# Kernel optimization log

Measured on AMD Instinct MI355X. Metric: run time of the kernel, lower is better.

## Reference

```python
import jax, jax.numpy as jnp
import numpy as np

B, SQ, SK, D, H, DFF, L = 8, 1024, 1024, 512, 8, 2048, 2
HD = D // H  # head dim = 64
EPS = 1e-5


def _ln(x, g, b):
    mu = jnp.mean(x, axis=-1, keepdims=True)
    var = jnp.mean((x - mu) ** 2, axis=-1, keepdims=True)
    return (x - mu) * jax.lax.rsqrt(var + EPS) * g + b


def setup_inputs() -> dict:
    key = jax.random.key(0)
    ks = jax.random.split(key, 16)
    std = 0.02
    inp = {
        'q': jax.random.normal(ks[0], (B, SQ, D), jnp.float32),
        'k': jax.random.normal(ks[1], (B, SK, D), jnp.float32),
        'v': jax.random.normal(ks[2], (B, SK, D), jnp.float32),
        # per-layer stacked params (weights stored [in, out])
        'WQ': jax.random.normal(ks[3], (L, D, D), jnp.float32) * std,
        'bQ': jnp.zeros((L, D), jnp.float32),
        'WK': jax.random.normal(ks[4], (L, D, D), jnp.float32) * std,
        'bK': jnp.zeros((L, D), jnp.float32),
        'WV': jax.random.normal(ks[5], (L, D, D), jnp.float32) * std,
        'bV': jnp.zeros((L, D), jnp.float32),
        'WO': jax.random.normal(ks[6], (L, D, D), jnp.float32) * std,
        'bO': jnp.zeros((L, D), jnp.float32),
        'Wf1': jax.random.normal(ks[7], (L, D, DFF), jnp.float32) * std,
        'bf1': jnp.zeros((L, DFF), jnp.float32),
        'Wf2': jax.random.normal(ks[8], (L, DFF, D), jnp.float32) * std,
        'bf2': jnp.zeros((L, D), jnp.float32),
        'ln1_g': jnp.ones((L, D), jnp.float32),
        'ln1_b': jnp.zeros((L, D), jnp.float32),
        'ln2_g': jnp.ones((L, D), jnp.float32),
        'ln2_b': jnp.zeros((L, D), jnp.float32),
        'scale': jnp.full((L,), HD ** -0.5, jnp.float32),       # self.scale init
        'extra_scale': jnp.ones((L,), jnp.float32),             # self.extra_scale init
        'gate_attn': jnp.ones((L,), jnp.float32),
        'gate_ffn': jnp.ones((L,), jnp.float32),
    }
    return inp


def reference(q, k, v, WQ, bQ, WK, bK, WV, bV, WO, bO, Wf1, bf1, Wf2, bf2,
              ln1_g, ln1_b, ln2_g, ln2_b, scale, extra_scale, gate_attn, gate_ffn):
    prev = None  # Realformer residual attention scores
    for i in range(L):
        # QKV projections -> [B, H, S, HD]
        qh = (jnp.einsum('bsd,de->bse', q, WQ[i]) + bQ[i]).reshape(B, SQ, H, HD).transpose(0, 2, 1, 3)
        kh = (jnp.einsum('bsd,de->bse', k, WK[i]) + bK[i]).reshape(B, SK, H, HD).transpose(0, 2, 1, 3)
        vh = (jnp.einsum('bsd,de->bse', v, WV[i]) + bV[i]).reshape(B, SK, H, HD).transpose(0, 2, 1, 3)
        eff_scale = scale[i] * jnp.clip(extra_scale[i], 0.01, 50.0)
        scores = jnp.einsum('bhqd,bhkd->bhqk', qh, kh) * eff_scale  # [B,H,SQ,SK]
        if prev is not None:
            scores = scores + prev
        attn = jax.nn.softmax(scores, axis=-1)
        out = jnp.einsum('bhqk,bhkd->bhqd', attn, vh)
        out = out.transpose(0, 2, 1, 3).reshape(B, SQ, D)
        out = jnp.einsum('bsd,de->bse', out, WO[i]) + bO[i]
        # gated residual + post-norm
        q = q + jax.nn.softplus(gate_attn[i]) * out
        q = _ln(q, ln1_g[i], ln1_b[i])
        # FFN (exact gelu like torch default)
        ff = jax.nn.gelu(jnp.einsum('bsd,df->bsf', q, Wf1[i]) + bf1[i], approximate=False)
        ff = jnp.einsum('bsf,fd->bsd', ff, Wf2[i]) + bf2[i]
        q = q + jax.nn.softplus(gate_ffn[i]) * ff
        q = _ln(q, ln2_g[i], ln2_b[i])
        prev = scores
    return q
```

## Files before the change

### kernel.cpp

```cpp
#include <hip/hip_runtime.h>

#define B_   8
#define SQ_  1024
#define SK_  1024
#define D_   512
#define H_   8
#define DFF_ 2048
#define L_   2
#define HD_  64
#define M_   8192

typedef __bf16 bf16;
using bf16x8 = __attribute__((ext_vector_type(8))) __bf16;
using f32x4  = __attribute__((ext_vector_type(4))) float;

__device__ inline f32x4 mfma16(bf16x8 a, bf16x8 b, f32x4 c) {
  return __builtin_amdgcn_mfma_f32_16x16x32_bf16(a, b, c, 0, 0, 0);
}

__device__ __forceinline__ void gl2lds16(const bf16* g, bf16* l) {
  __builtin_amdgcn_global_load_lds(
      (const __attribute__((address_space(1))) void*)g,
      (__attribute__((address_space(3))) void*)l, 16, 0, 0);
}

__global__ __launch_bounds__(256) void transpose_k(
    const float* __restrict__ in, bf16* __restrict__ out, int R, int C) {
  __shared__ bf16 tile[32][33];
  const float* inp  = in  + (size_t)blockIdx.z * R * C;
  bf16*        outp = out + (size_t)blockIdx.z * R * C;
  int c0 = blockIdx.x * 32, r0 = blockIdx.y * 32;
  int tx = threadIdx.x & 31, ty = threadIdx.x >> 5;
#pragma unroll
  for (int i = 0; i < 32; i += 8)
    tile[ty + i][tx] = (bf16)inp[(size_t)(r0 + ty + i) * C + c0 + tx];
  __syncthreads();
#pragma unroll
  for (int i = 0; i < 32; i += 8)
    outp[(size_t)(c0 + ty + i) * R + r0 + tx] = tile[tx][ty + i];
}

__global__ __launch_bounds__(256) void f2b_k(const float* __restrict__ in,
                                             bf16* __restrict__ out, int n) {
  int i = (blockIdx.x * 256 + threadIdx.x) * 4;
  if (i < n) {
    float4 v = *(const float4*)&in[i];
    out[i] = (bf16)v.x; out[i + 1] = (bf16)v.y;
    out[i + 2] = (bf16)v.z; out[i + 3] = (bf16)v.w;
  }
}

template<int BN>
__global__ __launch_bounds__(256) void gemm_t(
    const bf16* __restrict__ A, const bf16* __restrict__ Bt,
    const float* __restrict__ bias, bf16* __restrict__ Cb,
    float* __restrict__ Cf, int Nsz, int Ksz, int gelu) {
  constexpr int NI = BN / 32;
  __shared__ bf16 As[2][128 * 32];
  __shared__ bf16 Bs[2][BN * 32];
  const int tid = threadIdx.x;
  const int m0 = blockIdx.x * 128, n0 = blockIdx.y * BN;
  const int w = tid >> 6, lane = tid & 63, quad = lane >> 4, l16 = lane & 15;
  const int wm = (w & 1) << 6, wn = (w >> 1) * (BN / 2);
  const int r4 = lane >> 2;
  const int k8 = (lane & 3) * 8;
  f32x4 acc[4][NI] = {};

  auto stage = [&](int k0, int buf) {
    gl2lds16(&A[(size_t)(m0 + w * 16 + r4) * Ksz + k0 + k8],
             &As[buf][(w * 16) * 32]);
    gl2lds16(&A[(size_t)(m0 + (w + 4) * 16 + r4) * Ksz + k0 + k8],
             &As[buf][((w + 4) * 16) * 32]);
    gl2lds16(&Bt[(size_t)(n0 + w * 16 + r4) * Ksz + k0 + k8],
             &Bs[buf][(w * 16) * 32]);
    if constexpr (BN == 128)
      gl2lds16(&Bt[(size_t)(n0 + (w + 4) * 16 + r4) * Ksz + k0 + k8],
               &Bs[buf][((w + 4) * 16) * 32]);
  };

  stage(0, 0);
  __syncthreads();
  int buf = 0;
  for (int k0 = 0; k0 < Ksz; k0 += 32, buf ^= 1) {
    if (k0 + 32 < Ksz) stage(k0 + 32, buf ^ 1);
    bf16x8 af[4], bfr[NI];
#pragma unroll
    for (int i = 0; i < 4; i++)
      af[i] = *(const bf16x8*)&As[buf][(wm + i * 16 + l16) * 32 + quad * 8];
#pragma unroll
    for (int i = 0; i < NI; i++)
      bfr[i] = *(const bf16x8*)&Bs[buf][(wn + i * 16 + l16) * 32 + quad * 8];
#pragma unroll
    for (int mi = 0; mi < 4; mi++)
#pragma unroll
      for (int ni = 0; ni < NI; ni++)
        acc[mi][ni] = mfma16(af[mi], bfr[ni], acc[mi][ni]);
    __syncthreads();
  }
#pragma unroll
  for (int mi = 0; mi < 4; mi++)
#pragma unroll
    for (int ni = 0; ni < NI; ni++) {
      int col = n0 + wn + ni * 16 + l16;
      float bv = bias[col];
#pragma unroll
      for (int r = 0; r < 4; r++) {
        int row = m0 + wm + mi * 16 + quad * 4 + r;
        float x = acc[mi][ni][r] + bv;
        if (gelu) x = 0.5f * x * (1.0f + erff(x * 0.70710678118f));
        size_t idx = (size_t)row * Nsz + col;
        if (Cb) Cb[idx] = (bf16)x;
        if (Cf) Cf[idx] = x;
      }
    }
}

__global__ __launch_bounds__(256) void vtrans_k(const bf16* __restrict__ vh,
                                                int vstride, int coloff,
                                                bf16* __restrict__ vt) {
  __shared__ bf16 sm[64][72];
  int kt = blockIdx.x, bh = blockIdx.y;
  int b = bh >> 3, h = bh & 7;
  int tid = threadIdx.x;
  for (int c = tid; c < 512; c += 256) {
    int key = c >> 3, off = (c & 7) * 8;
    *(uint4*)&sm[key][off] = *(const uint4*)
        &vh[(size_t)(b * SK_ + kt * 64 + key) * vstride + coloff + h * 64 + off];
  }
  __syncthreads();
  for (int c = tid; c < 512; c += 256) {
    int hd = c >> 3, koff = (c & 7) * 8;
    bf16 tmp[8];
#pragma unroll
    for (int j = 0; j < 8; j++) tmp[j] = sm[koff + j][hd];
    *(uint4*)&vt[(size_t)(bh * 64 + hd) * SK_ + kt * 64 + koff] = *(uint4*)tmp;
  }
}

template<bool HAS0>
__global__ __launch_bounds__(256) void attn_t(
    const bf16* __restrict__ qh, const bf16* __restrict__ qh0,
    const bf16* __restrict__ kh, const bf16* __restrict__ kh0, int kstride,
    const bf16* __restrict__ vt, const float* __restrict__ scale,
    const float* __restrict__ extra, int li, bf16* __restrict__ ctx) {
  __shared__ bf16 Ks[2][2][64 * 32];
  __shared__ bf16 K0s[HAS0 ? 2 : 1][2][64 * 32];
  __shared__ bf16 Vs[2][2][64 * 32];
  __shared__ bf16 Ps[4][16 * 72];
  int qt = blockIdx.x, bh = blockIdx.y;
  int b = bh >> 3, h = bh & 7;
  int tid = threadIdx.x, w = tid >> 6, lane = tid & 63;
  int quad = lane >> 4, l16 = lane & 15;
  const int r4 = lane >> 2, c4 = (lane & 3) * 8;
  float eff1 = scale[li] * fminf(fmaxf(extra[li], 0.01f), 50.0f);
  float eff0 = HAS0 ? scale[li - 1] * fminf(fmaxf(extra[li - 1], 0.01f), 50.0f) : 0.f;
  int qrow = b * SQ_ + qt * 64 + w * 16 + l16;
  const bf16* qp = qh + (size_t)qrow * D_ + h * 64 + quad * 8;
  bf16x8 aq[2] = { *(const bf16x8*)qp, *(const bf16x8*)(qp + 32) };
#pragma unroll
  for (int k2 = 0; k2 < 2; k2++)
#pragma unroll
    for (int j = 0; j < 8; j++) aq[k2][j] = (bf16)((float)aq[k2][j] * eff1);
  bf16x8 aq0[2] = {};
  if constexpr (HAS0) {
    const bf16* qp0 = qh0 + (size_t)qrow * D_ + h * 64 + quad * 8;
    aq0[0] = *(const bf16x8*)qp0; aq0[1] = *(const bf16x8*)(qp0 + 32);
#pragma unroll
    for (int k2 = 0; k2 < 2; k2++)
#pragma unroll
      for (int j = 0; j < 8; j++) aq0[k2][j] = (bf16)((float)aq0[k2][j] * eff0);
  }
  bf16x8 ones;
#pragma unroll
  for (int j = 0; j < 8; j++) ones[j] = (bf16)1.0f;

  f32x4 o[4] = {};
  f32x4 ol = {};

  auto stage = [&](int kt, int bufi) {
    size_t kg = (size_t)(b * SK_ + kt * 64 + w * 16 + r4) * kstride + h * 64 + c4;
    gl2lds16(&kh[kg],      &Ks[bufi][0][(w * 16) * 32]);
    gl2lds16(&kh[kg + 32], &Ks[bufi][1][(w * 16) * 32]);
    if constexpr (HAS0) {
      gl2lds16(&kh0[kg],      &K0s[bufi][0][(w * 16) * 32]);
      gl2lds16(&kh0[kg + 32], &K0s[bufi][1][(w * 16) * 32]);
    }
    size_t vg = (size_t)(bh * 64 + w * 16 + r4) * SK_ + kt * 64 + c4;
    gl2lds16(&vt[vg],      &Vs[bufi][0][(w * 16) * 32]);
    gl2lds16(&vt[vg + 32], &Vs[bufi][1][(w * 16) * 32]);
  };

  stage(0, 0);
  __syncthreads();
  int buf = 0;
  for (int kt = 0; kt < SK_ / 64; kt++, buf ^= 1) {
    if (kt + 1 < SK_ / 64) stage(kt + 1, buf ^ 1);
#pragma unroll
    for (int ni = 0; ni < 4; ni++) {
      int ro = (ni * 16 + l16) * 32 + quad * 8;
      f32x4 t = {};
      t = mfma16(aq[0], *(const bf16x8*)&Ks[buf][0][ro], t);
      t = mfma16(aq[1], *(const bf16x8*)&Ks[buf][1][ro], t);
      if constexpr (HAS0) {
        t = mfma16(aq0[0], *(const bf16x8*)&K0s[buf][0][ro], t);
        t = mfma16(aq0[1], *(const bf16x8*)&K0s[buf][1][ro], t);
      }
#pragma unroll
      for (int r = 0; r < 4; r++)
        Ps[w][(quad * 4 + r) * 72 + ni * 16 + l16] = (bf16)__expf(t[r]);
    }
#pragma unroll
    for (int kk = 0; kk < 2; kk++) {
      bf16x8 ap = *(const bf16x8*)&Ps[w][l16 * 72 + quad * 8 + kk * 32];
      ol = mfma16(ap, ones, ol);
#pragma unroll
      for (int ni = 0; ni < 4; ni++) {
        bf16x8 bv = *(const bf16x8*)&Vs[buf][kk][(ni * 16 + l16) * 32 + quad * 8];
        o[ni] = mfma16(ap, bv, o[ni]);
      }
    }
    __syncthreads();
  }
#pragma unroll
  for (int ni = 0; ni < 4; ni++)
#pragma unroll
    for (int r = 0; r < 4; r++) {
      int row = b * SQ_ + qt * 64 + w * 16 + quad * 4 + r;
      ctx[(size_t)row * D_ + h * 64 + ni * 16 + l16] = (bf16)(o[ni][r] / ol[r]);
    }
}

__global__ __launch_bounds__(256) void ln_k(
    const float* __restrict__ cur_in, const float* __restrict__ add,
    const float* __restrict__ gate, const float* __restrict__ g,
    const float* __restrict__ bb, float* __restrict__ outf,
    bf16* __restrict__ outb) {
  int row = blockIdx.x, tid = threadIdx.x;
  float gv = gate[0];
  float sp = gv > 20.f ? gv : log1pf(expf(gv));
  size_t base = (size_t)row * D_;
  int c0 = tid * 2;
  float2 c2 = *(const float2*)&cur_in[base + c0];
  float2 a2 = *(const float2*)&add[base + c0];
  float x0 = c2.x + sp * a2.x, x1 = c2.y + sp * a2.y;
  float s = x0 + x1, s2 = x0 * x0 + x1 * x1;
#pragma unroll
  for (int m = 1; m < 64; m <<= 1) {
    s += __shfl_xor(s, m);
    s2 += __shfl_xor(s2, m);
  }
  __shared__ float sa[4], sb[4];
  int w = tid >> 6;
  if ((tid & 63) == 0) { sa[w] = s; sb[w] = s2; }
  __syncthreads();
  s = sa[0] + sa[1] + sa[2] + sa[3];
  s2 = sb[0] + sb[1] + sb[2] + sb[3];
  float mu = s * (1.f / D_);
  float var = s2 * (1.f / D_) - mu * mu;
  float rs = rsqrtf(var + 1e-5f);
  float y0 = (x0 - mu) * rs * g[c0] + bb[c0];
  float y1 = (x1 - mu) * rs * g[c0 + 1] + bb[c0 + 1];
  if (outf) { float2 y; y.x = y0; y.y = y1; *(float2*)&outf[base + c0] = y; }
  if (outb) { outb[base + c0] = (bf16)y0; outb[base + c0 + 1] = (bf16)y1; }
}

extern "C" void kernel_launch(void* const* d_in, const int* in_sizes, int n_in,
                              void* d_out, int out_size, void* d_ws,
                              size_t ws_size, hipStream_t stream) {
  const float* qin = (const float*)d_in[0];
  const float* kin = (const float*)d_in[1];
  const float* vin = (const float*)d_in[2];
  const float* WQ  = (const float*)d_in[3];
  const float* bQ  = (const float*)d_in[4];
  const float* WK  = (const float*)d_in[5];
  const float* bK  = (const float*)d_in[6];
  const float* WV  = (const float*)d_in[7];
  const float* bV  = (const float*)d_in[8];
  const float* WO  = (const float*)d_in[9];
  const float* bO  = (const float*)d_in[10];
  const float* Wf1 = (const float*)d_in[11];
  const float* bf1 = (const float*)d_in[12];
  const float* Wf2 = (const float*)d_in[13];
  const float* bf2 = (const float*)d_in[14];
  const float* l1g = (const float*)d_in[15];
  const float* l1b = (const float*)d_in[16];
  const float* l2g = (const float*)d_in[17];
  const float* l2b = (const float*)d_in[18];
  const float* sc  = (const float*)d_in[19];
  const float* ex  = (const float*)d_in[20];
  const float* ga  = (const float*)d_in[21];
  const float* gf  = (const float*)d_in[22];

  char* p = (char*)d_ws;
  auto alloc = [&](size_t bytes) {
    void* r = (void*)p;
    p += (bytes + 255) & ~(size_t)255;
    return r;
  };
  bf16* WQt  = (bf16*)alloc((size_t)L_ * D_ * D_ * 2);
  bf16* WKt  = (bf16*)alloc((size_t)L_ * D_ * D_ * 2);
  bf16* WVt  = (bf16*)alloc((size_t)L_ * D_ * D_ * 2);
  bf16* WOt  = (bf16*)alloc((size_t)L_ * D_ * D_ * 2);
  bf16* Wf1t = (bf16*)alloc((size_t)L_ * D_ * DFF_ * 2);
  bf16* Wf2t = (bf16*)alloc((size_t)L_ * D_ * DFF_ * 2);
  float* cur  = (float*)alloc((size_t)M_ * D_ * 4);
  bf16* curb  = (bf16*)alloc((size_t)M_ * D_ * 2);
  bf16* qb    = (bf16*)alloc((size_t)M_ * D_ * 2);
  bf16* kb    = (bf16*)alloc((size_t)M_ * D_ * 2);
  bf16* vb    = (bf16*)alloc((size_t)M_ * D_ * 2);
  bf16* khh   = (bf16*)alloc((size_t)M_ * 2 * D_ * 2);
  bf16* vhh   = (bf16*)alloc((size_t)M_ * 2 * D_ * 2);
  bf16* qh0b  = (bf16*)alloc((size_t)M_ * D_ * 2);
  bf16* qh1b  = (bf16*)alloc((size_t)M_ * D_ * 2);
  bf16* vt0   = (bf16*)alloc((size_t)M_ * D_ * 2);
  bf16* vt1   = (bf16*)alloc((size_t)M_ * D_ * 2);
  bf16* ctx   = (bf16*)alloc((size_t)M_ * D_ * 2);
  float* proj = (float*)alloc((size_t)M_ * D_ * 4);
  bf16* ffmid = (bf16*)alloc((size_t)M_ * DFF_ * 2);
  float* ffout = (float*)alloc((size_t)M_ * D_ * 4);

  transpose_k<<<dim3(D_ / 32, D_ / 32, L_), 256, 0, stream>>>(WQ, WQt, D_, D_);
  transpose_k<<<dim3(D_ / 32, D_ / 32, L_), 256, 0, stream>>>(WK, WKt, D_, D_);
  transpose_k<<<dim3(D_ / 32, D_ / 32, L_), 256, 0, stream>>>(WV, WVt, D_, D_);
  transpose_k<<<dim3(D_ / 32, D_ / 32, L_), 256, 0, stream>>>(WO, WOt, D_, D_);
  transpose_k<<<dim3(DFF_ / 32, D_ / 32, L_), 256, 0, stream>>>(Wf1, Wf1t, D_, DFF_);
  transpose_k<<<dim3(D_ / 32, DFF_ / 32, L_), 256, 0, stream>>>(Wf2, Wf2t, DFF_, D_);
  f2b_k<<<(M_ * D_) / 1024, 256, 0, stream>>>(qin, qb, M_ * D_);
  f2b_k<<<(M_ * D_) / 1024, 256, 0, stream>>>(kin, kb, M_ * D_);
  f2b_k<<<(M_ * D_) / 1024, 256, 0, stream>>>(vin, vb, M_ * D_);

  gemm_t<128><<<dim3(M_ / 128, 8), 256, 0, stream>>>(
      kb, WKt, bK, khh, nullptr, 2 * D_, D_, 0);
  gemm_t<128><<<dim3(M_ / 128, 8), 256, 0, stream>>>(
      vb, WVt, bV, vhh, nullptr, 2 * D_, D_, 0);
  vtrans_k<<<dim3(SK_ / 64, B_ * H_), 256, 0, stream>>>(vhh, 2 * D_, 0, vt0);
  vtrans_k<<<dim3(SK_ / 64, B_ * H_), 256, 0, stream>>>(vhh, 2 * D_, D_, vt1);
  gemm_t<64><<<dim3(M_ / 128, 8), 256, 0, stream>>>(
      qb, WQt, bQ, qh0b, nullptr, D_, D_, 0);

  for (int li = 0; li < L_; li++) {
    if (li > 0)
      gemm_t<64><<<dim3(M_ / 128, 8), 256, 0, stream>>>(
          curb, WQt + (size_t)li * D_ * D_, bQ + li * D_, qh1b, nullptr, D_, D_, 0);
    if (li == 0)
      attn_t<false><<<dim3(SQ_ / 64, B_ * H_), 256, 0, stream>>>(
          qh0b, qh0b, khh, khh, 2 * D_, vt0, sc, ex, 0, ctx);
    else
      attn_t<true><<<dim3(SQ_ / 64, B_ * H_), 256, 0, stream>>>(
          qh1b, qh0b, khh + (size_t)li * D_, khh, 2 * D_, vt1, sc, ex, 1, ctx);
    gemm_t<64><<<dim3(M_ / 128, 8), 256, 0, stream>>>(
        ctx, WOt + (size_t)li * D_ * D_, bO + li * D_, nullptr, proj, D_, D_, 0);
    ln_k<<<M_, 256, 0, stream>>>((li == 0) ? qin : cur, proj, ga + li,
                                 l1g + li * D_, l1b + li * D_, cur, curb);
    gemm_t<128><<<dim3(M_ / 128, DFF_ / 128), 256, 0, stream>>>(
        curb, Wf1t + (size_t)li * D_ * DFF_, bf1 + li * DFF_, ffmid, nullptr,
        DFF_, D_, 1);
    gemm_t<64><<<dim3(M_ / 128, 8), 256, 0, stream>>>(
        ffmid, Wf2t + (size_t)li * DFF_ * D_, bf2 + li * D_, nullptr, ffout,
        D_, DFF_, 0);
    ln_k<<<M_, 256, 0, stream>>>(cur, ffout, gf + li, l2g + li * D_,
                                 l2b + li * D_,
                                 (li == L_ - 1) ? (float*)d_out : cur,
                                 (li == L_ - 1) ? nullptr : curb);
  }
}
```

Baseline: 584.5 us.

## Double attention query tile per block and batch small preprocessing launches

The attention kernel now handles 128 query rows per block, two 16-row sub-tiles per wave, so each staged K/V tile in LDS is reused by twice as many queries. This halves the grid and the global K/V traffic. The P scratch row stride changes with the HAS0 variant. Separately, the four square weight transposes, the three fp32-to-bf16 casts and the two V transposes are each merged into a single launch to cut launch overhead. The price is more registers per thread and fewer blocks (512) to spread over the compute units.

```diff
diff --git a/kernel.cpp b/kernel.cpp
--- a/kernel.cpp
+++ b/kernel.cpp
@@ -24,6 +24,23 @@
       (__attribute__((address_space(3))) void*)l, 16, 0, 0);
 }
 
+struct TP4 { const float* in[4]; bf16* out[4]; };
+__global__ __launch_bounds__(256) void transpose4_k(TP4 p) {
+  __shared__ bf16 tile[32][33];
+  int z = blockIdx.z, wsel = z >> 1, l = z & 1;
+  const float* inp  = p.in[wsel]  + (size_t)l * D_ * D_;
+  bf16*        outp = p.out[wsel] + (size_t)l * D_ * D_;
+  int c0 = blockIdx.x * 32, r0 = blockIdx.y * 32;
+  int tx = threadIdx.x & 31, ty = threadIdx.x >> 5;
+#pragma unroll
+  for (int i = 0; i < 32; i += 8)
+    tile[ty + i][tx] = (bf16)inp[(size_t)(r0 + ty + i) * D_ + c0 + tx];
+  __syncthreads();
+#pragma unroll
+  for (int i = 0; i < 32; i += 8)
+    outp[(size_t)(c0 + ty + i) * D_ + r0 + tx] = tile[tx][ty + i];
+}
+
 __global__ __launch_bounds__(256) void transpose_k(
     const float* __restrict__ in, bf16* __restrict__ out, int R, int C) {
   __shared__ bf16 tile[32][33];
@@ -40,14 +57,17 @@
     outp[(size_t)(c0 + ty + i) * R + r0 + tx] = tile[tx][ty + i];
 }
 
-__global__ __launch_bounds__(256) void f2b_k(const float* __restrict__ in,
-                                             bf16* __restrict__ out, int n) {
+__global__ __launch_bounds__(256) void f2b3_k(
+    const float* __restrict__ a, const float* __restrict__ b,
+    const float* __restrict__ c, bf16* __restrict__ oa,
+    bf16* __restrict__ ob, bf16* __restrict__ oc) {
+  int which = blockIdx.y;
+  const float* in = (which == 0) ? a : (which == 1) ? b : c;
+  bf16* out = (which == 0) ? oa : (which == 1) ? ob : oc;
   int i = (blockIdx.x * 256 + threadIdx.x) * 4;
-  if (i < n) {
-    float4 v = *(const float4*)&in[i];
-    out[i] = (bf16)v.x; out[i + 1] = (bf16)v.y;
-    out[i + 2] = (bf16)v.z; out[i + 3] = (bf16)v.w;
-  }
+  float4 v = *(const float4*)&in[i];
+  out[i] = (bf16)v.x; out[i + 1] = (bf16)v.y;
+  out[i + 2] = (bf16)v.z; out[i + 3] = (bf16)v.w;
 }
 
 template<int BN>
@@ -115,17 +135,19 @@
     }
 }
 
-__global__ __launch_bounds__(256) void vtrans_k(const bf16* __restrict__ vh,
-                                                int vstride, int coloff,
-                                                bf16* __restrict__ vt) {
+__global__ __launch_bounds__(256) void vtrans2_k(const bf16* __restrict__ vhh,
+                                                 bf16* __restrict__ vt0,
+                                                 bf16* __restrict__ vt1) {
   __shared__ bf16 sm[64][72];
-  int kt = blockIdx.x, bh = blockIdx.y;
+  int kt = blockIdx.x, bh = blockIdx.y, z = blockIdx.z;
+  int coloff = z ? D_ : 0;
+  bf16* vt = z ? vt1 : vt0;
   int b = bh >> 3, h = bh & 7;
   int tid = threadIdx.x;
   for (int c = tid; c < 512; c += 256) {
     int key = c >> 3, off = (c & 7) * 8;
     *(uint4*)&sm[key][off] = *(const uint4*)
-        &vh[(size_t)(b * SK_ + kt * 64 + key) * vstride + coloff + h * 64 + off];
+        &vhh[(size_t)(b * SK_ + kt * 64 + key) * (2 * D_) + coloff + h * 64 + off];
   }
   __syncthreads();
   for (int c = tid; c < 512; c += 256) {
@@ -143,10 +165,11 @@
     const bf16* __restrict__ kh, const bf16* __restrict__ kh0, int kstride,
     const bf16* __restrict__ vt, const float* __restrict__ scale,
     const float* __restrict__ extra, int li, bf16* __restrict__ ctx) {
-  __shared__ bf16 Ks[2][2][64 * 32];
-  __shared__ bf16 K0s[HAS0 ? 2 : 1][2][64 * 32];
-  __shared__ bf16 Vs[2][2][64 * 32];
-  __shared__ bf16 Ps[4][16 * 72];
+  constexpr int PSTR = HAS0 ? 64 : 72;
+  __shared__ bf16 Ks[2 * 2 * 2048];
+  __shared__ bf16 K0s[HAS0 ? 2 * 2 * 2048 : 64];
+  __shared__ bf16 Vs[2 * 2 * 2048];
+  __shared__ bf16 Ps[4][32 * PSTR];
   int qt = blockIdx.x, bh = blockIdx.y;
   int b = bh >> 3, h = bh & 7;
   int tid = threadIdx.x, w = tid >> 6, lane = tid & 63;
@@ -154,40 +177,45 @@
   const int r4 = lane >> 2, c4 = (lane & 3) * 8;
   float eff1 = scale[li] * fminf(fmaxf(extra[li], 0.01f), 50.0f);
   float eff0 = HAS0 ? scale[li - 1] * fminf(fmaxf(extra[li - 1], 0.01f), 50.0f) : 0.f;
-  int qrow = b * SQ_ + qt * 64 + w * 16 + l16;
-  const bf16* qp = qh + (size_t)qrow * D_ + h * 64 + quad * 8;
-  bf16x8 aq[2] = { *(const bf16x8*)qp, *(const bf16x8*)(qp + 32) };
-#pragma unroll
-  for (int k2 = 0; k2 < 2; k2++)
-#pragma unroll
-    for (int j = 0; j < 8; j++) aq[k2][j] = (bf16)((float)aq[k2][j] * eff1);
-  bf16x8 aq0[2] = {};
-  if constexpr (HAS0) {
-    const bf16* qp0 = qh0 + (size_t)qrow * D_ + h * 64 + quad * 8;
-    aq0[0] = *(const bf16x8*)qp0; aq0[1] = *(const bf16x8*)(qp0 + 32);
+  bf16x8 aq[2][2], aq0[2][2];
+#pragma unroll
+  for (int mi = 0; mi < 2; mi++) {
+    int qrow = b * SQ_ + qt * 128 + w * 32 + mi * 16 + l16;
+    const bf16* qp = qh + (size_t)qrow * D_ + h * 64 + quad * 8;
+    aq[mi][0] = *(const bf16x8*)qp; aq[mi][1] = *(const bf16x8*)(qp + 32);
 #pragma unroll
     for (int k2 = 0; k2 < 2; k2++)
 #pragma unroll
-      for (int j = 0; j < 8; j++) aq0[k2][j] = (bf16)((float)aq0[k2][j] * eff0);
+      for (int j = 0; j < 8; j++)
+        aq[mi][k2][j] = (bf16)((float)aq[mi][k2][j] * eff1);
+    if constexpr (HAS0) {
+      const bf16* qp0 = qh0 + (size_t)qrow * D_ + h * 64 + quad * 8;
+      aq0[mi][0] = *(const bf16x8*)qp0; aq0[mi][1] = *(const bf16x8*)(qp0 + 32);
+#pragma unroll
+      for (int k2 = 0; k2 < 2; k2++)
+#pragma unroll
+        for (int j = 0; j < 8; j++)
+          aq0[mi][k2][j] = (bf16)((float)aq0[mi][k2][j] * eff0);
+    }
   }
   bf16x8 ones;
 #pragma unroll
   for (int j = 0; j < 8; j++) ones[j] = (bf16)1.0f;
 
-  f32x4 o[4] = {};
-  f32x4 ol = {};
+  f32x4 o[2][4] = {};
+  f32x4 ol[2] = {};
 
   auto stage = [&](int kt, int bufi) {
     size_t kg = (size_t)(b * SK_ + kt * 64 + w * 16 + r4) * kstride + h * 64 + c4;
-    gl2lds16(&kh[kg],      &Ks[bufi][0][(w * 16) * 32]);
-    gl2lds16(&kh[kg + 32], &Ks[bufi][1][(w * 16) * 32]);
+    gl2lds16(&kh[kg],      &Ks[(bufi * 2 + 0) * 2048 + (w * 16) * 32]);
+    gl2lds16(&kh[kg + 32], &Ks[(bufi * 2 + 1) * 2048 + (w * 16) * 32]);
     if constexpr (HAS0) {
-      gl2lds16(&kh0[kg],      &K0s[bufi][0][(w * 16) * 32]);
-      gl2lds16(&kh0[kg + 32], &K0s[bufi][1][(w * 16) * 32]);
+      gl2lds16(&kh0[kg],      &K0s[(bufi * 2 + 0) * 2048 + (w * 16) * 32]);
+      gl2lds16(&kh0[kg + 32], &K0s[(bufi * 2 + 1) * 2048 + (w * 16) * 32]);
     }
     size_t vg = (size_t)(bh * 64 + w * 16 + r4) * SK_ + kt * 64 + c4;
-    gl2lds16(&vt[vg],      &Vs[bufi][0][(w * 16) * 32]);
-    gl2lds16(&vt[vg + 32], &Vs[bufi][1][(w * 16) * 32]);
+    gl2lds16(&vt[vg],      &Vs[(bufi * 2 + 0) * 2048 + (w * 16) * 32]);
+    gl2lds16(&vt[vg + 32], &Vs[(bufi * 2 + 1) * 2048 + (w * 16) * 32]);
   };
 
   stage(0, 0);
@@ -196,38 +224,51 @@
   for (int kt = 0; kt < SK_ / 64; kt++, buf ^= 1) {
     if (kt + 1 < SK_ / 64) stage(kt + 1, buf ^ 1);
 #pragma unroll
-    for (int ni = 0; ni < 4; ni++) {
-      int ro = (ni * 16 + l16) * 32 + quad * 8;
-      f32x4 t = {};
-      t = mfma16(aq[0], *(const bf16x8*)&Ks[buf][0][ro], t);
-      t = mfma16(aq[1], *(const bf16x8*)&Ks[buf][1][ro], t);
-      if constexpr (HAS0) {
-        t = mfma16(aq0[0], *(const bf16x8*)&K0s[buf][0][ro], t);
-        t = mfma16(aq0[1], *(const bf16x8*)&K0s[buf][1][ro], t);
+    for (int mi = 0; mi < 2; mi++)
+#pragma unroll
+      for (int ni = 0; ni < 4; ni++) {
+        int ro = (ni * 16 + l16) * 32 + quad * 8;
+        f32x4 t = {};
+        t = mfma16(aq[mi][0], *(const bf16x8*)&Ks[0 * 2048 + buf * 4096 + ro], t);
+        t = mfma16(aq[mi][1], *(const bf16x8*)&Ks[1 * 2048 + buf * 4096 + ro], t);
+        if constexpr (HAS0) {
+          t = mfma16(aq0[mi][0], *(const bf16x8*)&K0s[0 * 2048 + buf * 4096 + ro], t);
+          t = mfma16(aq0[mi][1], *(const bf16x8*)&K0s[1 * 2048 + buf * 4096 + ro], t);
+        }
+#pragma unroll
+        for (int r = 0; r < 4; r++)
+          Ps[w][(mi * 16 + quad * 4 + r) * PSTR + ni * 16 + l16] =
+              (bf16)__expf(t[r]);
       }
 #pragma unroll
-      for (int r = 0; r < 4; r++)
-        Ps[w][(quad * 4 + r) * 72 + ni * 16 + l16] = (bf16)__expf(t[r]);
-    }
-#pragma unroll
     for (int kk = 0; kk < 2; kk++) {
-      bf16x8 ap = *(const bf16x8*)&Ps[w][l16 * 72 + quad * 8 + kk * 32];
-      ol = mfma16(ap, ones, ol);
-#pragma unroll
-      for (int ni = 0; ni < 4; ni++) {
-        bf16x8 bv = *(const bf16x8*)&Vs[buf][kk][(ni * 16 + l16) * 32 + quad * 8];
-        o[ni] = mfma16(ap, bv, o[ni]);
+      bf16x8 bv[4];
+#pragma unroll
+      for (int ni = 0; ni < 4; ni++)
+        bv[ni] = *(const bf16x8*)&Vs[kk * 2048 + buf * 4096 +
+                                     (ni * 16 + l16) * 32 + quad * 8];
+#pragma unroll
+      for (int mi = 0; mi < 2; mi++) {
+        bf16x8 ap = *(const bf16x8*)&Ps[w][(mi * 16 + l16) * PSTR +
+                                           kk * 32 + quad * 8];
+        ol[mi] = mfma16(ap, ones, ol[mi]);
+#pragma unroll
+        for (int ni = 0; ni < 4; ni++)
+          o[mi][ni] = mfma16(ap, bv[ni], o[mi][ni]);
       }
     }
     __syncthreads();
   }
 #pragma unroll
-  for (int ni = 0; ni < 4; ni++)
-#pragma unroll
-    for (int r = 0; r < 4; r++) {
-      int row = b * SQ_ + qt * 64 + w * 16 + quad * 4 + r;
-      ctx[(size_t)row * D_ + h * 64 + ni * 16 + l16] = (bf16)(o[ni][r] / ol[r]);
-    }
+  for (int mi = 0; mi < 2; mi++)
+#pragma unroll
+    for (int ni = 0; ni < 4; ni++)
+#pragma unroll
+      for (int r = 0; r < 4; r++) {
+        int row = b * SQ_ + qt * 128 + w * 32 + mi * 16 + quad * 4 + r;
+        ctx[(size_t)row * D_ + h * 64 + ni * 16 + l16] =
+            (bf16)(o[mi][ni][r] / ol[mi][r]);
+      }
 }
 
 __global__ __launch_bounds__(256) void ln_k(
@@ -319,22 +360,18 @@
   bf16* ffmid = (bf16*)alloc((size_t)M_ * DFF_ * 2);
   float* ffout = (float*)alloc((size_t)M_ * D_ * 4);
 
-  transpose_k<<<dim3(D_ / 32, D_ / 32, L_), 256, 0, stream>>>(WQ, WQt, D_, D_);
-  transpose_k<<<dim3(D_ / 32, D_ / 32, L_), 256, 0, stream>>>(WK, WKt, D_, D_);
-  transpose_k<<<dim3(D_ / 32, D_ / 32, L_), 256, 0, stream>>>(WV, WVt, D_, D_);
-  transpose_k<<<dim3(D_ / 32, D_ / 32, L_), 256, 0, stream>>>(WO, WOt, D_, D_);
+  TP4 tp; tp.in[0] = WQ; tp.in[1] = WK; tp.in[2] = WV; tp.in[3] = WO;
+  tp.out[0] = WQt; tp.out[1] = WKt; tp.out[2] = WVt; tp.out[3] = WOt;
+  transpose4_k<<<dim3(16, 16, 8), 256, 0, stream>>>(tp);
   transpose_k<<<dim3(DFF_ / 32, D_ / 32, L_), 256, 0, stream>>>(Wf1, Wf1t, D_, DFF_);
   transpose_k<<<dim3(D_ / 32, DFF_ / 32, L_), 256, 0, stream>>>(Wf2, Wf2t, DFF_, D_);
-  f2b_k<<<(M_ * D_) / 1024, 256, 0, stream>>>(qin, qb, M_ * D_);
-  f2b_k<<<(M_ * D_) / 1024, 256, 0, stream>>>(kin, kb, M_ * D_);
-  f2b_k<<<(M_ * D_) / 1024, 256, 0, stream>>>(vin, vb, M_ * D_);
+  f2b3_k<<<dim3((M_ * D_) / 1024, 3), 256, 0, stream>>>(qin, kin, vin, qb, kb, vb);
 
   gemm_t<128><<<dim3(M_ / 128, 8), 256, 0, stream>>>(
       kb, WKt, bK, khh, nullptr, 2 * D_, D_, 0);
   gemm_t<128><<<dim3(M_ / 128, 8), 256, 0, stream>>>(
       vb, WVt, bV, vhh, nullptr, 2 * D_, D_, 0);
-  vtrans_k<<<dim3(SK_ / 64, B_ * H_), 256, 0, stream>>>(vhh, 2 * D_, 0, vt0);
-  vtrans_k<<<dim3(SK_ / 64, B_ * H_), 256, 0, stream>>>(vhh, 2 * D_, D_, vt1);
+  vtrans2_k<<<dim3(SK_ / 64, B_ * H_, 2), 256, 0, stream>>>(vhh, vt0, vt1);
   gemm_t<64><<<dim3(M_ / 128, 8), 256, 0, stream>>>(
       qb, WQt, bQ, qh0b, nullptr, D_, D_, 0);
 
@@ -343,10 +380,10 @@
       gemm_t<64><<<dim3(M_ / 128, 8), 256, 0, stream>>>(
           curb, WQt + (size_t)li * D_ * D_, bQ + li * D_, qh1b, nullptr, D_, D_, 0);
     if (li == 0)
-      attn_t<false><<<dim3(SQ_ / 64, B_ * H_), 256, 0, stream>>>(
+      attn_t<false><<<dim3(SQ_ / 128, B_ * H_), 256, 0, stream>>>(
           qh0b, qh0b, khh, khh, 2 * D_, vt0, sc, ex, 0, ctx);
     else
-      attn_t<true><<<dim3(SQ_ / 64, B_ * H_), 256, 0, stream>>>(
+      attn_t<true><<<dim3(SQ_ / 128, B_ * H_), 256, 0, stream>>>(
           qh1b, qh0b, khh + (size_t)li * D_, khh, 2 * D_, vt1, sc, ex, 1, ctx);
     gemm_t<64><<<dim3(M_ / 128, 8), 256, 0, stream>>>(
         ctx, WOt + (size_t)li * D_ * D_, bO + li * D_, nullptr, proj, D_, D_, 0);
```

Result: faster. 550.4 us (-5.8%).
